# Performance work log

Hardware: AMD Instinct MI355X
Metric: run time of the kernel (lower is better)

## Reference

```python
import jax, jax.numpy as jnp
import numpy as np

N = 65536        # number of encoding vectors (flattened tokens)
K = 1024         # num_embeddings (codebook size)
D = 128          # embedding_dim
BETA = 0.25


def setup_inputs() -> dict:
    key = jax.random.key(0)
    k_enc, k_cb = jax.random.split(key)
    encoding = jax.random.normal(k_enc, (N, D), dtype=jnp.float32)
    # nn.Embedding weight initialized uniform(-1/K, 1/K)
    codebook = jax.random.uniform(k_cb, (K, D), dtype=jnp.float32,
                                  minval=-1.0 / K, maxval=1.0 / K)
    return {"encoding": encoding, "codebook": codebook}


def reference(encoding, codebook):
    # Nearest codebook entry per row. argmin of L2 distance == argmin of
    # squared distance; expand ||e - w||^2 = ||e||^2 - 2 e.w + ||w||^2.
    # ||e||^2 is constant per row, so it does not affect the argmin.
    scores = (-2.0 * jnp.einsum('nd,kd->nk', encoding, codebook)
              + jnp.sum(codebook * codebook, axis=-1)[None, :])  # [N, K]
    quantized_index = jnp.argmin(scores, axis=-1)                # [N] int
    quantized_embedding = codebook[quantized_index]              # [N, D] gather == onehot @ W

    sg = jax.lax.stop_gradient
    commitment_loss = jnp.mean((sg(quantized_embedding) - encoding) ** 2)
    embedding_loss = jnp.mean((quantized_embedding - sg(encoding)) ** 2)
    vq_loss = commitment_loss * BETA + embedding_loss

    # straight-through estimator
    quantized_st = encoding + sg(quantized_embedding - encoding)

    quantized_index = quantized_index[:, None]  # match torch unsqueeze(1) -> [N, 1]
    return (quantized_index, quantized_st, vq_loss, embedding_loss, commitment_loss)
```

## Files before the change

### kernel.cpp

```cpp
#include <hip/hip_runtime.h>


#define NROWS 65536
#define KCB   1024
#define DIM   128
#define DV    32
#define MSE_DENOM 8388608.0f
#define MARGIN 3.0e-5f
#define MARGINS 0.030720f
#define FLAGCAP 16384
#define CSCALE   1024.0f
#define CDESCALE 0.0009765625f

#define WS_CNORM_F  256
#define WS_CN1024_F 1280
#define WS_LIST_B   12288
#define WS_PH_B     77824
#define WS_NEEDED   339968

typedef __attribute__((ext_vector_type(16))) float float16v;
typedef _Float16 half8 __attribute__((ext_vector_type(8)));
union U4H8 { uint4 u; half8 h; };
union F4A  { float4 v; float f[4]; };
union F16V { float16v v; float f[16]; };
union HU   { _Float16 f; unsigned short u; };

__device__ __forceinline__ float fmed3(float a, float b, float c) {
  return __builtin_amdgcn_fmed3f(a, b, c);
}
__device__ __forceinline__ void gload16(const void* g, void* s) {
  __builtin_amdgcn_global_load_lds((const __attribute__((address_space(1))) unsigned int*)g,
                                   (__attribute__((address_space(3))) unsigned int*)s,
                                   16, 0, 0);
}

__global__ __launch_bounds__(256) void vq_prep_pack(const float* __restrict__ C,
                                                    float* __restrict__ wsf,
                                                    uint4* __restrict__ PH) {
  const int b = blockIdx.x;
  if (b < 64) {
    int g = b * 256 + threadIdx.x;
    int mt = g >> 9, s = (g >> 6) & 7, l = g & 63;
    int cw = mt * 32 + (l & 31);
    int k0 = s * 16 + (l >> 5) * 8;
    const float* src = C + (size_t)cw * DIM + k0;
    float4 x0 = *(const float4*)src;
    float4 x1 = *(const float4*)(src + 4);
    unsigned h[8];
    {
      float v[8] = {x0.x, x0.y, x0.z, x0.w, x1.x, x1.y, x1.z, x1.w};
#pragma unroll
      for (int j = 0; j < 8; ++j) { HU u; u.f = (_Float16)(CSCALE * v[j]); h[j] = u.u; }
    }
    PH[g] = make_uint4(h[0] | (h[1] << 16), h[2] | (h[3] << 16),
                       h[4] | (h[5] << 16), h[6] | (h[7] << 16));
  } else {
    int k = (b - 64) * 256 + threadIdx.x;
    if (k == 0) { wsf[0] = 0.0f; ((unsigned*)wsf)[1] = 0u; }
    const float4* c4 = (const float4*)C + (size_t)k * DV;
    float s = 0.f;
#pragma unroll 8
    for (int i = 0; i < DV; ++i) {
      float4 v = c4[i];
      s = fmaf(v.x, v.x, s); s = fmaf(v.y, v.y, s);
      s = fmaf(v.z, v.z, s); s = fmaf(v.w, v.w, s);
    }
    wsf[WS_CNORM_F + k]  = s;
    wsf[WS_CN1024_F + k] = s * CSCALE;
  }
}

__global__ __launch_bounds__(256, 3) void vq_main10(const float* __restrict__ E,
                                                    const float* __restrict__ C,
                                                    float* __restrict__ wsf,
                                                    float* __restrict__ out) {
  __shared__ uint4 SH[3][1024];
  __shared__ __align__(16) float CN[1024];
  __shared__ float X1[64], X2[64];
  __shared__ int   XI[64];
  __shared__ int   BI[64];

  const int tid  = threadIdx.x;
  const int w    = tid >> 6;
  const int l    = tid & 63;
  const int half = l >> 5;
  const int rr   = l & 31;
  const int pair = w >> 1;
  const int rw   = w & 1;
  const int row0 = blockIdx.x * 64;
  const int row  = row0 + rw * 32 + rr;

  const uint4* PHg = (const uint4*)((const char*)wsf + WS_PH_B);
  const uint4* CNg = (const uint4*)(wsf + WS_CN1024_F);

  half8 beh[8];
  float s2 = 0.f;
  const float* erow = E + (size_t)row * DIM + half * 8;
#pragma unroll
  for (int s = 0; s < 8; ++s) {
    float4 x0 = *(const float4*)(erow + s * 16);
    float4 x1 = *(const float4*)(erow + s * 16 + 4);
    float v[8] = {x0.x, x0.y, x0.z, x0.w, x1.x, x1.y, x1.z, x1.w};
#pragma unroll
    for (int j = 0; j < 8; ++j) {
      float y = v[j];
      s2 = fmaf(y, y, s2);
      beh[s][j] = (_Float16)(-2.f * y);
    }
  }
  __builtin_amdgcn_sched_barrier(0);

  gload16(CNg + tid, ((uint4*)CN) + tid);
  {
    const uint4* s0 = PHg;
    const uint4* s1 = PHg + 16 * 512;
    gload16(s0 + tid,       &SH[0][0] + tid);
    gload16(s0 + 256 + tid, &SH[0][0] + 256 + tid);
    gload16(s1 + tid,       &SH[0][0] + 512 + tid);
    gload16(s1 + 256 + tid, &SH[0][0] + 768 + tid);
    const uint4* t0 = PHg + 512;
    const uint4* t1 = PHg + 17 * 512;
    gload16(t0 + tid,       &SH[1][0] + tid);
    gload16(t0 + 256 + tid, &SH[1][0] + 256 + tid);
    gload16(t1 + tid,       &SH[1][0] + 512 + tid);
    gload16(t1 + 256 + tid, &SH[1][0] + 768 + tid);
  }
  __builtin_amdgcn_sched_barrier(0);

  float m1 = 3.0e38f, m2 = 3.0e38f;
  int   bi = 0;
  int   cur = 0, nxt = 2;

  for (int st = 0; st < 16; ++st) {
    if (st < 15) asm volatile("s_waitcnt vmcnt(4)" ::: "memory");
    else         asm volatile("s_waitcnt vmcnt(0)" ::: "memory");
    __builtin_amdgcn_s_barrier();
    asm volatile("" ::: "memory");

    if (st < 14) {
      const uint4* s0 = PHg + (size_t)(st + 2) * 512;
      const uint4* s1 = PHg + (size_t)(18 + st) * 512;
      uint4* nb = &SH[nxt][0];
      gload16(s0 + tid,       nb + tid);
      gload16(s0 + 256 + tid, nb + 256 + tid);
      gload16(s1 + tid,       nb + 512 + tid);
      gload16(s1 + 256 + tid, nb + 768 + tid);
    }

    const int tg = pair * 16 + st;
    F16V accA, accB;
#pragma unroll
    for (int q = 0; q < 4; ++q) {
      F4A c; c.v = *(const float4*)&CN[tg * 32 + q * 8 + half * 4];
      accA.f[q * 4 + 0] = c.f[0]; accA.f[q * 4 + 1] = c.f[1];
      accA.f[q * 4 + 2] = c.f[2]; accA.f[q * 4 + 3] = c.f[3];
    }
    accB.v = (float16v){0,0,0,0,0,0,0,0,0,0,0,0,0,0,0,0};
#pragma unroll
    for (int s = 0; s < 8; s += 2) {
      U4H8 h0, h1;
      h0.u = SH[cur][pair * 512 + s * 64 + l];
      h1.u = SH[cur][pair * 512 + (s + 1) * 64 + l];
      accA.v = __builtin_amdgcn_mfma_f32_32x32x16_f16(h0.h, beh[s],     accA.v, 0, 0, 0);
      accB.v = __builtin_amdgcn_mfma_f32_32x32x16_f16(h1.h, beh[s + 1], accB.v, 0, 0, 0);
    }

    const int kb = tg * 32 + half * 4;
#pragma unroll
    for (int reg = 0; reg < 16; ++reg) {
      float sc = accA.f[reg] + accB.f[reg];
      bool nb_ = sc < m1;
      m2 = fmed3(sc, m1, m2);
      m1 = fminf(sc, m1);
      bi = nb_ ? (kb + (reg >> 2) * 8 + (reg & 3)) : bi;
    }

    cur = (cur == 2) ? 0 : cur + 1;
    nxt = (nxt == 2) ? 0 : nxt + 1;
  }

  {
    float om1 = __shfl_xor(m1, 32, 64);
    float om2 = __shfl_xor(m2, 32, 64);
    int   obi = __shfl_xor(bi, 32, 64);
    float nsv = fminf(fminf(m2, om2), fmaxf(m1, om1));
    if (om1 < m1 || (om1 == m1 && obi < bi)) { m1 = om1; bi = obi; }
    m2 = nsv;
  }
  float en = s2 + __shfl_xor(s2, 32, 64);

  if (pair == 1 && half == 0) {
    X1[rw * 32 + rr] = m1; X2[rw * 32 + rr] = m2; XI[rw * 32 + rr] = bi;
  }
  __syncthreads();

  if (pair == 0 && half == 0) {
    const int r = rw * 32 + rr;
    float xb = X1[r], xs = X2[r];
    int   xi = XI[r];
    float sv = fminf(fminf(m2, xs), fmaxf(m1, xb));
    if (xb < m1 || (xb == m1 && xi < bi)) { m1 = xb; bi = xi; }
    out[row] = (float)bi;
    BI[r] = bi;
    if (sv - m1 < MARGINS) {
      unsigned idx = atomicAdd((unsigned*)wsf + 1, 1u);
      if (idx < FLAGCAP) ((int*)((char*)wsf + WS_LIST_B))[idx] = row;
    }
    float term = fmaf(m1, CDESCALE, en);
#pragma unroll
    for (int off = 16; off > 0; off >>= 1) term += __shfl_down(term, off);
    if (rr == 0) atomicAdd(wsf, term);
  }
  __syncthreads();

  const float4* C4   = (const float4*)C;
  float4*       out4 = (float4*)out;
#pragma unroll
  for (int it = 0; it < 8; ++it) {
    int flat = it * 256 + tid;
    int r = flat >> 5, d4 = flat & 31;
    out4[(NROWS / 4) + (size_t)(row0 + r) * DV + d4] = C4[(size_t)BI[r] * DV + d4];
  }
}

__global__ __launch_bounds__(256) void vq_fix(const float* __restrict__ E,
                                              const float* __restrict__ C,
                                              float* __restrict__ wsf,
                                              float* __restrict__ out) {
  __shared__ float4 eL[4][32];
  __shared__ float  RV[4][4];
  __shared__ int    RI[4][4];
  __shared__ int    RESi[4];
  const int tid = threadIdx.x;
  const int wv  = tid >> 6;
  const int ln  = tid & 63;

  if (blockIdx.x == 0 && tid == 0) {
    float mse = wsf[0] / MSE_DENOM;
    out[NROWS + NROWS * DIM + 0] = 1.25f * mse;
    out[NROWS + NROWS * DIM + 1] = mse;
    out[NROWS + NROWS * DIM + 2] = mse;
  }

  const int* list = (const int*)((const char*)wsf + WS_LIST_B);
  int nf = (int)((const unsigned*)wsf)[1];
  if (nf > FLAGCAP) nf = FLAGCAP;
  const float4* E4 = (const float4*)E;
  const float4* C4 = (const float4*)C;
  const float*  cn = wsf + WS_CNORM_F;
  float4* out4 = (float4*)out;

  for (int g = blockIdx.x; g * 4 < nf; g += gridDim.x) {
    const int base = g * 4;
    if (tid < 128) {
      int r = tid >> 5, d4 = tid & 31;
      int R = (base + r < nf) ? list[base + r] : list[base];
      eL[r][d4] = E4[(size_t)R * DV + d4];
    }
    __syncthreads();
    float bv[4] = {3.0e38f, 3.0e38f, 3.0e38f, 3.0e38f};
    int   bi[4] = {0, 0, 0, 0};
#pragma unroll
    for (int j = 0; j < 4; ++j) {
      int k = j * 256 + tid;
      float d0 = 0.f, d1 = 0.f, d2 = 0.f, d3 = 0.f;
#pragma unroll 4
      for (int d4 = 0; d4 < 32; ++d4) {
        float4 c = C4[(size_t)k * DV + d4];
        float4 e0 = eL[0][d4], e1 = eL[1][d4], e2 = eL[2][d4], e3 = eL[3][d4];
        d0 = fmaf(c.x, e0.x, d0); d0 = fmaf(c.y, e0.y, d0);
        d0 = fmaf(c.z, e0.z, d0); d0 = fmaf(c.w, e0.w, d0);
        d1 = fmaf(c.x, e1.x, d1); d1 = fmaf(c.y, e1.y, d1);
        d1 = fmaf(c.z, e1.z, d1); d1 = fmaf(c.w, e1.w, d1);
        d2 = fmaf(c.x, e2.x, d2); d2 = fmaf(c.y, e2.y, d2);
        d2 = fmaf(c.z, e2.z, d2); d2 = fmaf(c.w, e2.w, d2);
        d3 = fmaf(c.x, e3.x, d3); d3 = fmaf(c.y, e3.y, d3);
        d3 = fmaf(c.w, e3.w, d3); d3 = fmaf(c.z, e3.z, d3);
      }
      float cnk = cn[k];
      float s0 = fmaf(-2.f, d0, cnk);
      float s1 = fmaf(-2.f, d1, cnk);
      float s2 = fmaf(-2.f, d2, cnk);
      float s3 = fmaf(-2.f, d3, cnk);
      if (s0 < bv[0] || (s0 == bv[0] && k < bi[0])) { bv[0] = s0; bi[0] = k; }
      if (s1 < bv[1] || (s1 == bv[1] && k < bi[1])) { bv[1] = s1; bi[1] = k; }
      if (s2 < bv[2] || (s2 == bv[2] && k < bi[2])) { bv[2] = s2; bi[2] = k; }
      if (s3 < bv[3] || (s3 == bv[3] && k < bi[3])) { bv[3] = s3; bi[3] = k; }
    }
#pragma unroll
    for (int off = 32; off > 0; off >>= 1) {
#pragma unroll
      for (int r = 0; r < 4; ++r) {
        float wv_ = __shfl_down(bv[r], off);
        int   ji  = __shfl_down(bi[r], off);
        if (wv_ < bv[r] || (wv_ == bv[r] && ji < bi[r])) { bv[r] = wv_; bi[r] = ji; }
      }
    }
    if (ln == 0) {
#pragma unroll
      for (int r = 0; r < 4; ++r) { RV[wv][r] = bv[r]; RI[wv][r] = bi[r]; }
    }
    __syncthreads();
    if (tid < 4) {
      float v = RV[0][tid]; int i = RI[0][tid];
#pragma unroll
      for (int q = 1; q < 4; ++q) {
        float vv = RV[q][tid]; int ii = RI[q][tid];
        if (vv < v || (vv == v && ii < i)) { v = vv; i = ii; }
      }
      RESi[tid] = i;
      if (base + tid < nf) out[list[base + tid]] = (float)i;
    }
    __syncthreads();
    if (tid < 128) {
      int r = tid >> 5, d4 = tid & 31;
      if (base + r < nf) {
        int R = list[base + r];
        out4[(NROWS / 4) + (size_t)R * DV + d4] = C4[(size_t)RESi[r] * DV + d4];
      }
    }
    __syncthreads();
  }
}

__global__ __launch_bounds__(256) void vq_prep_fb(const float* __restrict__ C,
                                                  float* __restrict__ ws) {
  int k = blockIdx.x * 256 + threadIdx.x;
  if (k == 0) ws[0] = 0.0f;
  const float4* c4 = (const float4*)C + (size_t)k * DV;
  float s = 0.f;
#pragma unroll 8
  for (int i = 0; i < DV; ++i) {
    float4 v = c4[i];
    s = fmaf(v.x, v.x, s); s = fmaf(v.y, v.y, s);
    s = fmaf(v.z, v.z, s); s = fmaf(v.w, v.w, s);
  }
  ws[64 + k] = s;
}

__global__ __launch_bounds__(256) void vq_main_fb(const float* __restrict__ E,
                                                  const float* __restrict__ C,
                                                  const float* __restrict__ cnorm,
                                                  float* __restrict__ out,
                                                  float* __restrict__ lossacc) {
  __shared__ float smem[16384];
  float4* EsV = (float4*)smem;
  float4* CsV = (float4*)(smem + 8192);
  const int tid  = threadIdx.x;
  const int row0 = blockIdx.x * 64;
#pragma unroll
  for (int i = 0; i < 8; ++i) {
    int flat = i * 256 + tid;
    int r = flat >> 5, d4 = flat & 31;
    EsV[r * 32 + (d4 ^ (r & 31))] = ((const float4*)E)[(size_t)(row0 + r) * DV + d4];
  }
  const int tx = tid & 15, ty = tid >> 4;
  int rbase[4], rmask[4];
#pragma unroll
  for (int i = 0; i < 4; ++i) { int r = i * 16 + ty; rbase[i] = r * 32; rmask[i] = r & 31; }
  float bestv[4]; int besti[4];
#pragma unroll
  for (int i = 0; i < 4; ++i) { bestv[i] = 3.0e38f; besti[i] = 0; }
  for (int ch = 0; ch < 16; ++ch) {
    const int k0 = ch * 64;
    __syncthreads();
#pragma unroll
    for (int i = 0; i < 8; ++i) {
      int flat = i * 256 + tid;
      int k = flat >> 5, d4 = flat & 31;
      CsV[k * 32 + (d4 ^ (k & 31))] = ((const float4*)C)[(size_t)(k0 + k) * DV + d4];
    }
    __syncthreads();
    float acc[4][4] = {};
#pragma unroll 8
    for (int d4 = 0; d4 < DV; ++d4) {
      float4 a[4], b[4];
#pragma unroll
      for (int i = 0; i < 4; ++i) a[i] = EsV[rbase[i] + (d4 ^ rmask[i])];
#pragma unroll
      for (int j = 0; j < 4; ++j) { int k = j * 16 + tx; b[j] = CsV[k * 32 + (d4 ^ (k & 31))]; }
#pragma unroll
      for (int i = 0; i < 4; ++i)
#pragma unroll
        for (int j = 0; j < 4; ++j) {
          acc[i][j] = fmaf(a[i].x, b[j].x, acc[i][j]);
          acc[i][j] = fmaf(a[i].y, b[j].y, acc[i][j]);
          acc[i][j] = fmaf(a[i].z, b[j].z, acc[i][j]);
          acc[i][j] = fmaf(a[i].w, b[j].w, acc[i][j]);
        }
    }
#pragma unroll
    for (int j = 0; j < 4; ++j) {
      int kg = k0 + j * 16 + tx;
      float cnv = cnorm[kg];
#pragma unroll
      for (int i = 0; i < 4; ++i) {
        float s = fmaf(-2.0f, acc[i][j], cnv);
        if (s < bestv[i] || (s == bestv[i] && kg < besti[i])) { bestv[i] = s; besti[i] = kg; }
      }
    }
  }
  float* Rv = smem + 8192;
  int*   Ri = (int*)(smem + 9216);
  int*   BIf = (int*)(smem + 10240);
  __syncthreads();
#pragma unroll
  for (int i = 0; i < 4; ++i) {
    int r = i * 16 + ty;
    Rv[r * 16 + tx] = bestv[i];
    Ri[r * 16 + tx] = besti[i];
  }
  __syncthreads();
  if (tid < 64) {
    const int r = tid;
    float bv = Rv[r * 16]; int bi = Ri[r * 16];
#pragma unroll
    for (int t = 1; t < 16; ++t) {
      float v = Rv[r * 16 + t]; int ii = Ri[r * 16 + t];
      if (v < bv || (v == bv && ii < bi)) { bv = v; bi = ii; }
    }
    float en = 0.f;
#pragma unroll 8
    for (int d4 = 0; d4 < DV; ++d4) {
      float4 v = EsV[r * 32 + (d4 ^ (r & 31))];
      en = fmaf(v.x, v.x, en); en = fmaf(v.y, v.y, en);
      en = fmaf(v.z, v.z, en); en = fmaf(v.w, v.w, en);
    }
    out[row0 + r] = (float)bi;
    BIf[r] = bi;
    float blocksum = en + bv;
#pragma unroll
    for (int off = 32; off > 0; off >>= 1) blocksum += __shfl_down(blocksum, off);
    if (tid == 0) atomicAdd(lossacc, blocksum);
  }
  __syncthreads();
  const float4* C4   = (const float4*)C;
  float4*       out4 = (float4*)out;
  for (int flat = tid; flat < 64 * DV; flat += 256) {
    int r = flat >> 5, d4 = flat & 31;
    out4[(NROWS / 4) + (size_t)(row0 + r) * DV + d4] = C4[(size_t)BIf[r] * DV + d4];
  }
}

__global__ void vq_final_fb(const float* __restrict__ ws, float* __restrict__ out) {
  if (threadIdx.x == 0 && blockIdx.x == 0) {
    float mse = ws[0] / MSE_DENOM;
    out[NROWS + NROWS * DIM + 0] = 1.25f * mse;
    out[NROWS + NROWS * DIM + 1] = mse;
    out[NROWS + NROWS * DIM + 2] = mse;
  }
}

extern "C" void kernel_launch(void* const* d_in, const int* in_sizes, int n_in,
                              void* d_out, int out_size, void* d_ws, size_t ws_size,
                              hipStream_t stream) {
  const float* E = (const float*)d_in[0];
  const float* C = (const float*)d_in[1];
  float* out = (float*)d_out;
  float* wsf = (float*)d_ws;

  if (ws_size >= (size_t)WS_NEEDED) {
    uint4* PH = (uint4*)((char*)d_ws + WS_PH_B);
    vq_prep_pack<<<68, 256, 0, stream>>>(C, wsf, PH);
    vq_main10<<<NROWS / 64, 256, 0, stream>>>(E, C, wsf, out);
    vq_fix<<<512, 256, 0, stream>>>(E, C, wsf, out);
  } else {
    vq_prep_fb<<<4, 256, 0, stream>>>(C, wsf);
    vq_main_fb<<<NROWS / 64, 256, 0, stream>>>(E, C, wsf + 64, out, wsf);
    vq_final_fb<<<1, 64, 0, stream>>>(wsf, out);
  }
}
```

Before: 163.4 us.

## Read packed codebook directly from global/L2 instead of LDS-staged pipeline

The main kernel no longer stages packed fp16 codebook tiles into LDS through a triple-buffered global_load_lds pipeline with per-step barriers. Each wave now scans all 1024 codewords for its own 32 rows, loading MFMA operands and codebook norms straight from global memory (expected to stay L2-resident). Blocks now cover 128 rows with four independent waves, which removes the cross-wave merge through shared memory and most barriers. In exchange, every wave issues its own global loads for the full codebook, so the kernel relies on cache bandwidth and has less latency hiding, with occupancy lowered to 2 blocks per SIMD hint.

```diff
diff --git a/kernel.cpp b/kernel.cpp
--- a/kernel.cpp
+++ b/kernel.cpp
@@ -27,11 +27,6 @@
 
 __device__ __forceinline__ float fmed3(float a, float b, float c) {
   return __builtin_amdgcn_fmed3f(a, b, c);
-}
-__device__ __forceinline__ void gload16(const void* g, void* s) {
-  __builtin_amdgcn_global_load_lds((const __attribute__((address_space(1))) unsigned int*)g,
-                                   (__attribute__((address_space(3))) unsigned int*)s,
-                                   16, 0, 0);
 }
 
 __global__ __launch_bounds__(256) void vq_prep_pack(const float* __restrict__ C,
@@ -70,28 +65,22 @@
   }
 }
 
-__global__ __launch_bounds__(256, 3) void vq_main10(const float* __restrict__ E,
+__global__ __launch_bounds__(256, 2) void vq_main11(const float* __restrict__ E,
                                                     const float* __restrict__ C,
                                                     float* __restrict__ wsf,
                                                     float* __restrict__ out) {
-  __shared__ uint4 SH[3][1024];
-  __shared__ __align__(16) float CN[1024];
-  __shared__ float X1[64], X2[64];
-  __shared__ int   XI[64];
-  __shared__ int   BI[64];
+  __shared__ int BI[128];
 
   const int tid  = threadIdx.x;
   const int w    = tid >> 6;
   const int l    = tid & 63;
   const int half = l >> 5;
   const int rr   = l & 31;
-  const int pair = w >> 1;
-  const int rw   = w & 1;
-  const int row0 = blockIdx.x * 64;
-  const int row  = row0 + rw * 32 + rr;
-
-  const uint4* PHg = (const uint4*)((const char*)wsf + WS_PH_B);
-  const uint4* CNg = (const uint4*)(wsf + WS_CN1024_F);
+  const int row0 = blockIdx.x * 128;
+  const int row  = row0 + w * 32 + rr;
+
+  const uint4*  PHg = (const uint4*)((const char*)wsf + WS_PH_B);
+  const float4* CNb = (const float4*)(wsf + WS_CN1024_F);
 
   half8 beh[8];
   float s2 = 0.f;
@@ -108,62 +97,36 @@
       beh[s][j] = (_Float16)(-2.f * y);
     }
   }
-  __builtin_amdgcn_sched_barrier(0);
-
-  gload16(CNg + tid, ((uint4*)CN) + tid);
-  {
-    const uint4* s0 = PHg;
-    const uint4* s1 = PHg + 16 * 512;
-    gload16(s0 + tid,       &SH[0][0] + tid);
-    gload16(s0 + 256 + tid, &SH[0][0] + 256 + tid);
-    gload16(s1 + tid,       &SH[0][0] + 512 + tid);
-    gload16(s1 + 256 + tid, &SH[0][0] + 768 + tid);
-    const uint4* t0 = PHg + 512;
-    const uint4* t1 = PHg + 17 * 512;
-    gload16(t0 + tid,       &SH[1][0] + tid);
-    gload16(t0 + 256 + tid, &SH[1][0] + 256 + tid);
-    gload16(t1 + tid,       &SH[1][0] + 512 + tid);
-    gload16(t1 + 256 + tid, &SH[1][0] + 768 + tid);
-  }
-  __builtin_amdgcn_sched_barrier(0);
 
   float m1 = 3.0e38f, m2 = 3.0e38f;
   int   bi = 0;
-  int   cur = 0, nxt = 2;
-
-  for (int st = 0; st < 16; ++st) {
-    if (st < 15) asm volatile("s_waitcnt vmcnt(4)" ::: "memory");
-    else         asm volatile("s_waitcnt vmcnt(0)" ::: "memory");
-    __builtin_amdgcn_s_barrier();
-    asm volatile("" ::: "memory");
-
-    if (st < 14) {
-      const uint4* s0 = PHg + (size_t)(st + 2) * 512;
-      const uint4* s1 = PHg + (size_t)(18 + st) * 512;
-      uint4* nb = &SH[nxt][0];
-      gload16(s0 + tid,       nb + tid);
-      gload16(s0 + 256 + tid, nb + 256 + tid);
-      gload16(s1 + tid,       nb + 512 + tid);
-      gload16(s1 + 256 + tid, nb + 768 + tid);
-    }
-
-    const int tg = pair * 16 + st;
+
+#pragma unroll 4
+  for (int tg = 0; tg < 32; ++tg) {
+    const uint4* src = PHg + (size_t)tg * 512 + l;
+    U4H8 h0, h1, h2, h3, h4, h5, h6, h7;
+    h0.u = src[0];   h1.u = src[64];  h2.u = src[128]; h3.u = src[192];
+    h4.u = src[256]; h5.u = src[320]; h6.u = src[384]; h7.u = src[448];
+
+    const float4* cn = CNb + tg * 8 + half;
+    F4A c0, c1, c2, c3;
+    c0.v = cn[0]; c1.v = cn[2]; c2.v = cn[4]; c3.v = cn[6];
+
     F16V accA, accB;
-#pragma unroll
-    for (int q = 0; q < 4; ++q) {
-      F4A c; c.v = *(const float4*)&CN[tg * 32 + q * 8 + half * 4];
-      accA.f[q * 4 + 0] = c.f[0]; accA.f[q * 4 + 1] = c.f[1];
-      accA.f[q * 4 + 2] = c.f[2]; accA.f[q * 4 + 3] = c.f[3];
-    }
+    accA.f[0]  = c0.f[0]; accA.f[1]  = c0.f[1]; accA.f[2]  = c0.f[2]; accA.f[3]  = c0.f[3];
+    accA.f[4]  = c1.f[0]; accA.f[5]  = c1.f[1]; accA.f[6]  = c1.f[2]; accA.f[7]  = c1.f[3];
+    accA.f[8]  = c2.f[0]; accA.f[9]  = c2.f[1]; accA.f[10] = c2.f[2]; accA.f[11] = c2.f[3];
+    accA.f[12] = c3.f[0]; accA.f[13] = c3.f[1]; accA.f[14] = c3.f[2]; accA.f[15] = c3.f[3];
     accB.v = (float16v){0,0,0,0,0,0,0,0,0,0,0,0,0,0,0,0};
-#pragma unroll
-    for (int s = 0; s < 8; s += 2) {
-      U4H8 h0, h1;
-      h0.u = SH[cur][pair * 512 + s * 64 + l];
-      h1.u = SH[cur][pair * 512 + (s + 1) * 64 + l];
-      accA.v = __builtin_amdgcn_mfma_f32_32x32x16_f16(h0.h, beh[s],     accA.v, 0, 0, 0);
-      accB.v = __builtin_amdgcn_mfma_f32_32x32x16_f16(h1.h, beh[s + 1], accB.v, 0, 0, 0);
-    }
+
+    accA.v = __builtin_amdgcn_mfma_f32_32x32x16_f16(h0.h, beh[0], accA.v, 0, 0, 0);
+    accB.v = __builtin_amdgcn_mfma_f32_32x32x16_f16(h1.h, beh[1], accB.v, 0, 0, 0);
+    accA.v = __builtin_amdgcn_mfma_f32_32x32x16_f16(h2.h, beh[2], accA.v, 0, 0, 0);
+    accB.v = __builtin_amdgcn_mfma_f32_32x32x16_f16(h3.h, beh[3], accB.v, 0, 0, 0);
+    accA.v = __builtin_amdgcn_mfma_f32_32x32x16_f16(h4.h, beh[4], accA.v, 0, 0, 0);
+    accB.v = __builtin_amdgcn_mfma_f32_32x32x16_f16(h5.h, beh[5], accB.v, 0, 0, 0);
+    accA.v = __builtin_amdgcn_mfma_f32_32x32x16_f16(h6.h, beh[6], accA.v, 0, 0, 0);
+    accB.v = __builtin_amdgcn_mfma_f32_32x32x16_f16(h7.h, beh[7], accB.v, 0, 0, 0);
 
     const int kb = tg * 32 + half * 4;
 #pragma unroll
@@ -174,9 +137,6 @@
       m1 = fminf(sc, m1);
       bi = nb_ ? (kb + (reg >> 2) * 8 + (reg & 3)) : bi;
     }
-
-    cur = (cur == 2) ? 0 : cur + 1;
-    nxt = (nxt == 2) ? 0 : nxt + 1;
   }
 
   {
@@ -189,20 +149,11 @@
   }
   float en = s2 + __shfl_xor(s2, 32, 64);
 
-  if (pair == 1 && half == 0) {
-    X1[rw * 32 + rr] = m1; X2[rw * 32 + rr] = m2; XI[rw * 32 + rr] = bi;
-  }
-  __syncthreads();
-
-  if (pair == 0 && half == 0) {
-    const int r = rw * 32 + rr;
-    float xb = X1[r], xs = X2[r];
-    int   xi = XI[r];
-    float sv = fminf(fminf(m2, xs), fmaxf(m1, xb));
-    if (xb < m1 || (xb == m1 && xi < bi)) { m1 = xb; bi = xi; }
+  if (half == 0) {
+    const int r = w * 32 + rr;
     out[row] = (float)bi;
     BI[r] = bi;
-    if (sv - m1 < MARGINS) {
+    if (m2 - m1 < MARGINS) {
       unsigned idx = atomicAdd((unsigned*)wsf + 1, 1u);
       if (idx < FLAGCAP) ((int*)((char*)wsf + WS_LIST_B))[idx] = row;
     }
@@ -216,7 +167,7 @@
   const float4* C4   = (const float4*)C;
   float4*       out4 = (float4*)out;
 #pragma unroll
-  for (int it = 0; it < 8; ++it) {
+  for (int it = 0; it < 16; ++it) {
     int flat = it * 256 + tid;
     int r = flat >> 5, d4 = flat & 31;
     out4[(NROWS / 4) + (size_t)(row0 + r) * DV + d4] = C4[(size_t)BI[r] * DV + d4];
@@ -275,7 +226,7 @@
         d2 = fmaf(c.x, e2.x, d2); d2 = fmaf(c.y, e2.y, d2);
         d2 = fmaf(c.z, e2.z, d2); d2 = fmaf(c.w, e2.w, d2);
         d3 = fmaf(c.x, e3.x, d3); d3 = fmaf(c.y, e3.y, d3);
-        d3 = fmaf(c.w, e3.w, d3); d3 = fmaf(c.z, e3.z, d3);
+        d3 = fmaf(c.z, e3.z, d3); d3 = fmaf(c.w, e3.w, d3);
       }
       float cnk = cn[k];
       float s0 = fmaf(-2.f, d0, cnk);
@@ -462,7 +413,7 @@
   if (ws_size >= (size_t)WS_NEEDED) {
     uint4* PH = (uint4*)((char*)d_ws + WS_PH_B);
     vq_prep_pack<<<68, 256, 0, stream>>>(C, wsf, PH);
-    vq_main10<<<NROWS / 64, 256, 0, stream>>>(E, C, wsf, out);
+    vq_main11<<<NROWS / 128, 256, 0, stream>>>(E, C, wsf, out);
     vq_fix<<<512, 256, 0, stream>>>(E, C, wsf, out);
   } else {
     vq_prep_fb<<<4, 256, 0, stream>>>(C, wsf);
```

Result: no change. 165.2 us (+1.1%).
